# Kernel tuning notes

Measured on AMD Instinct MI355X. Metric: run time of the kernel, lower is better.

## Reference

```python
import jax, jax.numpy as jnp
import numpy as np

B, C, K = 8192, 4096, 4096
BK, BN = 1, 16          # block-sparse tile sizes (bk x bn)
KEEP = 0.3


def setup_inputs() -> dict:
    key = jax.random.key(0)
    kx, kw, kb, km = jax.random.split(key, 4)
    stdv = 1.0 / np.sqrt(C * K)  # reset_parameters uses 1/sqrt(C*K)
    x = jax.random.normal(kx, (B, C), dtype=jnp.float32)
    weight = jax.random.uniform(kw, (K, C), dtype=jnp.float32, minval=-stdv, maxval=stdv)
    # block mask on (K/bk, C/bn) grid, expanded to full weight shape
    blk = (jax.random.uniform(km, (K // BK, C // BN)) < KEEP).astype(jnp.float32)
    mask = jnp.repeat(jnp.repeat(blk, BK, axis=0), BN, axis=1)  # [K, C]
    weight = weight * mask
    bias = jax.random.uniform(kb, (K,), dtype=jnp.float32, minval=-stdv, maxval=stdv)
    return {"x": x, "weight": weight, "bias": bias}


def reference(x, weight, bias):
    # SparseLinearRelu forward (sparse-kernel path, attr='relu'):
    # y = relu(x @ W^T + b); zero blocks of W contribute nothing (skipped by kernel).
    return jax.nn.relu(jnp.dot(x, weight.T) + bias)
```

## Files before the change

kernel.cpp:

```cpp
#include <hip/hip_runtime.h>
#include <hip/hip_bf16.h>

typedef __attribute__((ext_vector_type(4))) float f32x4;
typedef __attribute__((ext_vector_type(8))) short bf16x8;
typedef __attribute__((ext_vector_type(4))) short bf16x4v;

#define M_DIM 8192
#define N_DIM 4096
#define K_DIM 4096
#define NX (M_DIM * K_DIM)
#define NW (N_DIM * K_DIM)

#define BM 256
#define BN 256
#define BK 64
#define NKT (K_DIM / BK)
#define THREADS 512

#define GLOAD_LDS16(g, l)                                                        \
  __builtin_amdgcn_global_load_lds(                                              \
      (const __attribute__((address_space(1))) void*)(g),                        \
      (__attribute__((address_space(3))) void*)(l), 16, 0, 0)

__global__ __launch_bounds__(256) void convert_bf16(const float* __restrict__ x,
                                                    const float* __restrict__ w,
                                                    short* __restrict__ ws) {
  const long stride = (long)gridDim.x * blockDim.x;
  const long total8 = ((long)NX + NW) / 8;
  for (long i = blockIdx.x * (long)blockDim.x + threadIdx.x; i < total8; i += stride) {
    const long base = i * 8;
    const float* src = (base < NX) ? (x + base) : (w + (base - NX));
    short* dst = ws + base;
    f32x4 a = *(const f32x4*)src;
    f32x4 b = *(const f32x4*)(src + 4);
    bf16x8 o;
    o[0] = (short)__bfloat16_as_ushort(__float2bfloat16(a[0]));
    o[1] = (short)__bfloat16_as_ushort(__float2bfloat16(a[1]));
    o[2] = (short)__bfloat16_as_ushort(__float2bfloat16(a[2]));
    o[3] = (short)__bfloat16_as_ushort(__float2bfloat16(a[3]));
    o[4] = (short)__bfloat16_as_ushort(__float2bfloat16(b[0]));
    o[5] = (short)__bfloat16_as_ushort(__float2bfloat16(b[1]));
    o[6] = (short)__bfloat16_as_ushort(__float2bfloat16(b[2]));
    o[7] = (short)__bfloat16_as_ushort(__float2bfloat16(b[3]));
    *(bf16x8*)dst = o;
  }
}

__global__ __launch_bounds__(THREADS, 2) void gemm256_bf16(
    const short* __restrict__ Abf,
    const short* __restrict__ Bbf,
    const float* __restrict__ bias,
    float* __restrict__ Y) {
  __shared__ short lds[2 * 32768];
  char* const ldsb = (char*)lds;

  const int tid  = threadIdx.x;
  const int lane = tid & 63;
  const int wave = tid >> 6;
  const int wm   = wave >> 2;
  const int wn   = wave & 3;

  const int lin = blockIdx.x + blockIdx.y * (N_DIM / BN);
  const int swz = (lin & 7) * 64 + (lin >> 3);
  const int bx = swz & 15;
  const int by = swz >> 4;
  const long rowA0 = (long)by * BM;
  const long rowB0 = (long)bx * BN;

  const int sg_col = (((lane & 7) ^ ((lane >> 3) & 7)) << 3);
  const int s_row  = wave * 8 + (lane >> 3);
  const int voff = s_row * K_DIM + sg_col;

  const short* uA = Abf + rowA0 * (long)K_DIM;
  const short* uB = Bbf + rowB0 * (long)K_DIM;

  const int offk0 = (lane & 15) * 128 + ((((lane >> 4)) ^ (lane & 7)) << 4);
  const int offk1 = (lane & 15) * 128 + (((4 + (lane >> 4)) ^ (lane & 7)) << 4);

#define STAGE_HALF(BOFF_, HALF_, TT) do {                                        \
    const short* u_ = ((HALF_) < 2 ? uA : uB) +                                  \
                      (long)(((HALF_) & 1) * 128) * K_DIM + (long)(TT) * BK;     \
    char* l_ = ldsb + (BOFF_) + ((HALF_) < 2 ? 0 : 32768) +                      \
               ((HALF_) & 1) * 16384 + wave * 1024;                              \
    GLOAD_LDS16(u_ + voff, l_);                                                  \
    GLOAD_LDS16(u_ + 64 * K_DIM + voff, l_ + 8192);                              \
  } while (0)

#define PH_READ_A(DST, BOFF_, MADD) do {                                         \
    const char* pa_ = ldsb + (BOFF_) + wm * 16384 + (MADD);                      \
    _Pragma("unroll")                                                            \
    for (int m_ = 0; m_ < 4; ++m_) {                                             \
      DST[m_][0] = *(const bf16x8*)(pa_ + m_ * 2048 + offk0);                    \
      DST[m_][1] = *(const bf16x8*)(pa_ + m_ * 2048 + offk1);                    \
    }                                                                            \
  } while (0)

#define PH_READ_B(DST, BOFF_, NADD) do {                                         \
    const char* pb_ = ldsb + (BOFF_) + 32768 + wn * 8192 + (NADD);               \
    _Pragma("unroll")                                                            \
    for (int n_ = 0; n_ < 2; ++n_) {                                             \
      DST[n_][0] = *(const bf16x8*)(pb_ + n_ * 2048 + offk0);                    \
      DST[n_][1] = *(const bf16x8*)(pb_ + n_ * 2048 + offk1);                    \
    }                                                                            \
  } while (0)

#define MFMA16(AF, BF, MB, NB) do {                                              \
    __builtin_amdgcn_s_setprio(1);                                               \
    _Pragma("unroll")                                                            \
    for (int kk_ = 0; kk_ < 2; ++kk_)                                            \
      _Pragma("unroll")                                                          \
      for (int m_ = 0; m_ < 4; ++m_)                                             \
        _Pragma("unroll")                                                        \
        for (int n_ = 0; n_ < 2; ++n_)                                           \
          acc[(MB) + m_][(NB) + n_] = __builtin_amdgcn_mfma_f32_16x16x32_bf16(   \
              AF[m_][kk_], BF[n_][kk_], acc[(MB) + m_][(NB) + n_], 0, 0, 0);     \
    __builtin_amdgcn_s_setprio(0);                                               \
  } while (0)

#define TILE(BOFF_, T, DO_ST, VM) do {                                           \
                               \
    PH_READ_A(af, BOFF_, 0);                                                     \
    PH_READ_B(bfr01, BOFF_, 0);                                                  \
    MFMA16(af, bfr01, 0, 0);                                                     \
    __builtin_amdgcn_s_barrier();                                                \
                                        \
    PH_READ_B(bfr23, BOFF_, 4096);                                               \
    MFMA16(af, bfr23, 0, 2);                                                     \
    __builtin_amdgcn_s_barrier();                                                \
                                        \
    PH_READ_A(af, BOFF_, 8192);                                                  \
    MFMA16(af, bfr01, 4, 0);                                                     \
    __builtin_amdgcn_s_barrier();                                                \
               \
    if (DO_ST) {                                                                 \
      STAGE_HALF(BOFF_, 0, (T) + 2);                                             \
      STAGE_HALF(BOFF_, 1, (T) + 2);                                             \
      STAGE_HALF(BOFF_, 2, (T) + 2);                                             \
      STAGE_HALF(BOFF_, 3, (T) + 2);                                             \
    }                                                                            \
    MFMA16(af, bfr23, 4, 2);                                                     \
    if ((VM) == 8)      asm volatile("s_waitcnt vmcnt(8)" ::: "memory");         \
    else if ((VM) == 0) asm volatile("s_waitcnt vmcnt(0)" ::: "memory");         \
    if ((VM) >= 0) __builtin_amdgcn_s_barrier();                                 \
  } while (0)

  f32x4 acc[8][4];
#pragma unroll
  for (int i = 0; i < 8; ++i)
#pragma unroll
    for (int j = 0; j < 4; ++j) acc[i][j] = (f32x4)0.0f;

  bf16x8 af[4][2], bfr01[2][2], bfr23[2][2];

  STAGE_HALF(0, 0, 0);
  STAGE_HALF(0, 1, 0);
  STAGE_HALF(0, 2, 0);
  STAGE_HALF(0, 3, 0);
  STAGE_HALF(65536, 0, 1);
  STAGE_HALF(65536, 1, 1);
  STAGE_HALF(65536, 2, 1);
  STAGE_HALF(65536, 3, 1);
  asm volatile("s_waitcnt vmcnt(8)" ::: "memory");
  __builtin_amdgcn_s_barrier();

  for (int tp = 0; tp < NKT / 2 - 1; ++tp) {
    const int t0 = 2 * tp;
    TILE(0,     t0,     1, 8);
    TILE(65536, t0 + 1, 1, 8);
  }
  TILE(0,     NKT - 2, 0, 0);
  TILE(65536, NKT - 1, 0, -1);

#undef TILE
#undef MFMA16
#undef PH_READ_B
#undef PH_READ_A
#undef STAGE_HALF

  const int c0 = lane & 15;
  const int r0 = (lane >> 4) * 4;
#pragma unroll
  for (int j = 0; j < 4; ++j) {
    const long gc = rowB0 + wn * 64 + j * 16 + c0;
    const float bv = bias[gc];
#pragma unroll
    for (int i = 0; i < 8; ++i) {
      const long gr0 = rowA0 + wm * 128 + i * 16 + r0;
#pragma unroll
      for (int r = 0; r < 4; ++r) {
        float v = acc[i][j][r] + bv;
        Y[(gr0 + r) * (long)N_DIM + gc] = fmaxf(v, 0.0f);
      }
    }
  }
}

#define FBM 128
#define FBK 32
#define FLDSS 40
__global__ __launch_bounds__(256) void fallback_gemm(
    const float* __restrict__ X, const float* __restrict__ W,
    const float* __restrict__ bias, float* __restrict__ Y) {
  __shared__ short As[FBM * FLDSS];
  __shared__ short Bs[FBM * FLDSS];
  const int tid = threadIdx.x, lane = tid & 63, wave = tid >> 6;
  const int wm = (wave >> 1) * 64, wn = (wave & 1) * 64;
  const long rowA0 = (long)blockIdx.y * FBM, rowB0 = (long)blockIdx.x * FBM;
  const int srow = tid >> 3, scol = (tid & 7) * 4;
  const float* Aptr = X + (rowA0 + srow) * (long)K_DIM + scol;
  const float* Bptr = W + (rowB0 + srow) * (long)K_DIM + scol;
  f32x4 ra[4], rb[4];
#pragma unroll
  for (int i = 0; i < 4; ++i) {
    ra[i] = *(const f32x4*)(Aptr + (long)i * 32 * K_DIM);
    rb[i] = *(const f32x4*)(Bptr + (long)i * 32 * K_DIM);
  }
  f32x4 acc[4][4];
#pragma unroll
  for (int i = 0; i < 4; ++i)
#pragma unroll
    for (int j = 0; j < 4; ++j) acc[i][j] = (f32x4)0.0f;
  for (int kt = 0; kt < K_DIM / FBK; ++kt) {
    __syncthreads();
#pragma unroll
    for (int i = 0; i < 4; ++i) {
      bf16x4v pa, pb;
#pragma unroll
      for (int j = 0; j < 4; ++j) {
        pa[j] = (short)__bfloat16_as_ushort(__float2bfloat16(ra[i][j]));
        pb[j] = (short)__bfloat16_as_ushort(__float2bfloat16(rb[i][j]));
      }
      *(bf16x4v*)&As[(i * 32 + srow) * FLDSS + scol] = pa;
      *(bf16x4v*)&Bs[(i * 32 + srow) * FLDSS + scol] = pb;
    }
    if (kt + 1 < K_DIM / FBK) {
      const float* An = Aptr + (kt + 1) * FBK;
      const float* Bn = Bptr + (kt + 1) * FBK;
#pragma unroll
      for (int i = 0; i < 4; ++i) {
        ra[i] = *(const f32x4*)(An + (long)i * 32 * K_DIM);
        rb[i] = *(const f32x4*)(Bn + (long)i * 32 * K_DIM);
      }
    }
    __syncthreads();
    bf16x8 af[4], bfr[4];
#pragma unroll
    for (int i = 0; i < 4; ++i) {
      af[i]  = *(const bf16x8*)&As[(wm + i * 16 + (lane & 15)) * FLDSS + (lane >> 4) * 8];
      bfr[i] = *(const bf16x8*)&Bs[(wn + i * 16 + (lane & 15)) * FLDSS + (lane >> 4) * 8];
    }
#pragma unroll
    for (int i = 0; i < 4; ++i)
#pragma unroll
      for (int j = 0; j < 4; ++j)
        acc[i][j] = __builtin_amdgcn_mfma_f32_16x16x32_bf16(af[i], bfr[j], acc[i][j], 0, 0, 0);
  }
  const int r0 = (lane >> 4) * 4, c0 = lane & 15;
#pragma unroll
  for (int j = 0; j < 4; ++j) {
    const long gc = rowB0 + wn + j * 16 + c0;
    const float bv = bias[gc];
#pragma unroll
    for (int i = 0; i < 4; ++i) {
      const long gr0 = rowA0 + wm + i * 16 + r0;
#pragma unroll
      for (int r = 0; r < 4; ++r) {
        float v = acc[i][j][r] + bv;
        Y[(gr0 + r) * (long)N_DIM + gc] = fmaxf(v, 0.0f);
      }
    }
  }
}

extern "C" void kernel_launch(void* const* d_in, const int* in_sizes, int n_in,
                              void* d_out, int out_size, void* d_ws, size_t ws_size,
                              hipStream_t stream) {
  const float* x = (const float*)d_in[0];
  const float* w = (const float*)d_in[1];
  const float* b = (const float*)d_in[2];
  float* y = (float*)d_out;

  const size_t need = (size_t)(NX + NW) * sizeof(short);
  if (ws_size >= need) {
    short* ws = (short*)d_ws;
    convert_bf16<<<2048, 256, 0, stream>>>(x, w, ws);
    dim3 grid(N_DIM / BN, M_DIM / BM);
    gemm256_bf16<<<grid, dim3(THREADS), 0, stream>>>(ws, ws + NX, b, y);
  } else {
    dim3 grid(N_DIM / FBM, M_DIM / FBM);
    fallback_gemm<<<grid, dim3(256), 0, stream>>>(x, w, b, y);
  }
}
```

Baseline: 296.5 us.

## Switch main GEMM to 32x32x16 bf16 MFMA with reworked fragment reads

Replaces the 16x16x32 MFMA tiling with 32x32x16 MFMA instructions. LDS fragment offsets, A/B register fragments, the accumulator layout and the epilogue store mapping are all changed to match. The global-to-LDS staging for the next tile is split across two phases of the tile loop instead of being issued all at once. Larger MFMA tiles cut the LDS reads per FLOP and the instruction count, but the new swizzled offsets may cause bank conflicts, and the 32x32 output layout makes the epilogue stores more scattered.

```diff
diff --git a/kernel.cpp b/kernel.cpp
--- a/kernel.cpp
+++ b/kernel.cpp
@@ -2,6 +2,7 @@
 #include <hip/hip_bf16.h>
 
 typedef __attribute__((ext_vector_type(4))) float f32x4;
+typedef __attribute__((ext_vector_type(16))) float f32x16;
 typedef __attribute__((ext_vector_type(8))) short bf16x8;
 typedef __attribute__((ext_vector_type(4))) short bf16x4v;
 
@@ -74,8 +75,10 @@
   const short* uA = Abf + rowA0 * (long)K_DIM;
   const short* uB = Bbf + rowB0 * (long)K_DIM;
 
-  const int offk0 = (lane & 15) * 128 + ((((lane >> 4)) ^ (lane & 7)) << 4);
-  const int offk1 = (lane & 15) * 128 + (((4 + (lane >> 4)) ^ (lane & 7)) << 4);
+  int offs[4];
+#pragma unroll
+  for (int s = 0; s < 4; ++s)
+    offs[s] = (lane & 31) * 128 + ((((2 * s) | (lane >> 5)) ^ (lane & 7)) << 4);
 
 #define STAGE_HALF(BOFF_, HALF_, TT) do {                                        \
     const short* u_ = ((HALF_) < 2 ? uA : uB) +                                  \
@@ -86,71 +89,63 @@
     GLOAD_LDS16(u_ + 64 * K_DIM + voff, l_ + 8192);                              \
   } while (0)
 
-#define PH_READ_A(DST, BOFF_, MADD) do {                                         \
-    const char* pa_ = ldsb + (BOFF_) + wm * 16384 + (MADD);                      \
+#define READ_A2(DST, BOFF_, MTB) do {                                            \
+    const char* pa_ = ldsb + (BOFF_) + wm * 16384 + (MTB) * 4096;                \
     _Pragma("unroll")                                                            \
-    for (int m_ = 0; m_ < 4; ++m_) {                                             \
-      DST[m_][0] = *(const bf16x8*)(pa_ + m_ * 2048 + offk0);                    \
-      DST[m_][1] = *(const bf16x8*)(pa_ + m_ * 2048 + offk1);                    \
-    }                                                                            \
-  } while (0)
-
-#define PH_READ_B(DST, BOFF_, NADD) do {                                         \
-    const char* pb_ = ldsb + (BOFF_) + 32768 + wn * 8192 + (NADD);               \
+    for (int mt_ = 0; mt_ < 2; ++mt_)                                            \
+      _Pragma("unroll")                                                          \
+      for (int s_ = 0; s_ < 4; ++s_)                                             \
+        DST[mt_][s_] = *(const bf16x8*)(pa_ + mt_ * 4096 + offs[s_]);            \
+  } while (0)
+
+#define READ_B1(DST, BOFF_, NT) do {                                             \
+    const char* pb_ = ldsb + (BOFF_) + 32768 + wn * 8192 + (NT) * 4096;          \
     _Pragma("unroll")                                                            \
-    for (int n_ = 0; n_ < 2; ++n_) {                                             \
-      DST[n_][0] = *(const bf16x8*)(pb_ + n_ * 2048 + offk0);                    \
-      DST[n_][1] = *(const bf16x8*)(pb_ + n_ * 2048 + offk1);                    \
-    }                                                                            \
-  } while (0)
-
-#define MFMA16(AF, BF, MB, NB) do {                                              \
+    for (int s_ = 0; s_ < 4; ++s_)                                               \
+      DST[s_] = *(const bf16x8*)(pb_ + offs[s_]);                                \
+  } while (0)
+
+#define MFMA8(AF2, BF, MT0, NT) do {                                             \
     __builtin_amdgcn_s_setprio(1);                                               \
     _Pragma("unroll")                                                            \
-    for (int kk_ = 0; kk_ < 2; ++kk_)                                            \
+    for (int s_ = 0; s_ < 4; ++s_)                                               \
       _Pragma("unroll")                                                          \
-      for (int m_ = 0; m_ < 4; ++m_)                                             \
-        _Pragma("unroll")                                                        \
-        for (int n_ = 0; n_ < 2; ++n_)                                           \
-          acc[(MB) + m_][(NB) + n_] = __builtin_amdgcn_mfma_f32_16x16x32_bf16(   \
-              AF[m_][kk_], BF[n_][kk_], acc[(MB) + m_][(NB) + n_], 0, 0, 0);     \
+      for (int mt_ = 0; mt_ < 2; ++mt_)                                          \
+        acc[(MT0) + mt_][NT] = __builtin_amdgcn_mfma_f32_32x32x16_bf16(          \
+            AF2[mt_][s_], BF[s_], acc[(MT0) + mt_][NT], 0, 0, 0);                \
     __builtin_amdgcn_s_setprio(0);                                               \
   } while (0)
 
 #define TILE(BOFF_, T, DO_ST, VM) do {                                           \
                                \
-    PH_READ_A(af, BOFF_, 0);                                                     \
-    PH_READ_B(bfr01, BOFF_, 0);                                                  \
-    MFMA16(af, bfr01, 0, 0);                                                     \
+    READ_A2(af01, BOFF_, 0);                                                     \
+    READ_B1(bf0, BOFF_, 0);                                                      \
+    MFMA8(af01, bf0, 0, 0);                                                      \
     __builtin_amdgcn_s_barrier();                                                \
-                                        \
-    PH_READ_B(bfr23, BOFF_, 4096);                                               \
-    MFMA16(af, bfr23, 0, 2);                                                     \
+                                       \
+    READ_A2(af23, BOFF_, 2);                                                     \
+    MFMA8(af23, bf0, 2, 0);                                                      \
     __builtin_amdgcn_s_barrier();                                                \
-                                        \
-    PH_READ_A(af, BOFF_, 8192);                                                  \
-    MFMA16(af, bfr01, 4, 0);                                                     \
+                           \
+    READ_B1(bf1, BOFF_, 1);                                                      \
+    if (DO_ST) { STAGE_HALF(BOFF_, 0, (T) + 2); STAGE_HALF(BOFF_, 1, (T) + 2); } \
+    MFMA8(af23, bf1, 2, 1);                                                      \
     __builtin_amdgcn_s_barrier();                                                \
-               \
-    if (DO_ST) {                                                                 \
-      STAGE_HALF(BOFF_, 0, (T) + 2);                                             \
-      STAGE_HALF(BOFF_, 1, (T) + 2);                                             \
-      STAGE_HALF(BOFF_, 2, (T) + 2);                                             \
-      STAGE_HALF(BOFF_, 3, (T) + 2);                                             \
-    }                                                                            \
-    MFMA16(af, bfr23, 4, 2);                                                     \
+                   \
+    if (DO_ST) { STAGE_HALF(BOFF_, 2, (T) + 2); STAGE_HALF(BOFF_, 3, (T) + 2); } \
+    MFMA8(af01, bf1, 0, 1);                                                      \
     if ((VM) == 8)      asm volatile("s_waitcnt vmcnt(8)" ::: "memory");         \
     else if ((VM) == 0) asm volatile("s_waitcnt vmcnt(0)" ::: "memory");         \
     if ((VM) >= 0) __builtin_amdgcn_s_barrier();                                 \
   } while (0)
 
-  f32x4 acc[8][4];
-#pragma unroll
-  for (int i = 0; i < 8; ++i)
-#pragma unroll
-    for (int j = 0; j < 4; ++j) acc[i][j] = (f32x4)0.0f;
-
-  bf16x8 af[4][2], bfr01[2][2], bfr23[2][2];
+  f32x16 acc[4][2];
+#pragma unroll
+  for (int i = 0; i < 4; ++i)
+#pragma unroll
+    for (int j = 0; j < 2; ++j) acc[i][j] = (f32x16)0.0f;
+
+  bf16x8 af01[2][4], af23[2][4], bf0[4], bf1[4];
 
   STAGE_HALF(0, 0, 0);
   STAGE_HALF(0, 1, 0);
@@ -172,24 +167,25 @@
   TILE(65536, NKT - 1, 0, -1);
 
 #undef TILE
-#undef MFMA16
-#undef PH_READ_B
-#undef PH_READ_A
+#undef MFMA8
+#undef READ_B1
+#undef READ_A2
 #undef STAGE_HALF
 
-  const int c0 = lane & 15;
-  const int r0 = (lane >> 4) * 4;
-#pragma unroll
-  for (int j = 0; j < 4; ++j) {
-    const long gc = rowB0 + wn * 64 + j * 16 + c0;
+  const int c0 = lane & 31;
+  const int r0 = 4 * (lane >> 5);
+#pragma unroll
+  for (int nt = 0; nt < 2; ++nt) {
+    const long gc = rowB0 + wn * 64 + nt * 32 + c0;
     const float bv = bias[gc];
 #pragma unroll
-    for (int i = 0; i < 8; ++i) {
-      const long gr0 = rowA0 + wm * 128 + i * 16 + r0;
-#pragma unroll
-      for (int r = 0; r < 4; ++r) {
-        float v = acc[i][j][r] + bv;
-        Y[(gr0 + r) * (long)N_DIM + gc] = fmaxf(v, 0.0f);
+    for (int mt = 0; mt < 4; ++mt) {
+      const long gr0 = rowA0 + wm * 128 + mt * 32 + r0;
+#pragma unroll
+      for (int r = 0; r < 16; ++r) {
+        const long gr = gr0 + (r & 3) + 8 * (r >> 2);
+        float v = acc[mt][nt][r] + bv;
+        Y[gr * (long)N_DIM + gc] = fmaxf(v, 0.0f);
       }
     }
   }
```

New measurement: 283.9 us. -4.3%, faster.

## Split next-tile staging across phases and vectorize epilogue stores via LDS transpose

Applied to the files above, without the earlier changes.

The global-to-LDS staging of the tile two steps ahead is split in two. Half is issued after the second A-fragment read and half just before the last MFMA group, which spreads memory traffic across the compute phases. The prologue staging order is changed to match. The epilogue now routes each wave's accumulators through a per-wave LDS scratch area so lanes can write 16-byte row-contiguous float4 stores with a vectorized bias add, replacing scattered 4-byte stores. This trades extra LDS traffic and some scratch reuse risk for fewer, better-coalesced global writes.

```diff
diff --git a/kernel.cpp b/kernel.cpp
--- a/kernel.cpp
+++ b/kernel.cpp
@@ -127,17 +127,13 @@
     PH_READ_B(bfr23, BOFF_, 4096);                                               \
     MFMA16(af, bfr23, 0, 2);                                                     \
     __builtin_amdgcn_s_barrier();                                                \
-                                        \
+                          \
     PH_READ_A(af, BOFF_, 8192);                                                  \
+    if (DO_ST) { STAGE_HALF(BOFF_, 2, (T) + 2); STAGE_HALF(BOFF_, 3, (T) + 2); } \
     MFMA16(af, bfr01, 4, 0);                                                     \
     __builtin_amdgcn_s_barrier();                                                \
-               \
-    if (DO_ST) {                                                                 \
-      STAGE_HALF(BOFF_, 0, (T) + 2);                                             \
-      STAGE_HALF(BOFF_, 1, (T) + 2);                                             \
-      STAGE_HALF(BOFF_, 2, (T) + 2);                                             \
-      STAGE_HALF(BOFF_, 3, (T) + 2);                                             \
-    }                                                                            \
+                   \
+    if (DO_ST) { STAGE_HALF(BOFF_, 0, (T) + 2); STAGE_HALF(BOFF_, 1, (T) + 2); } \
     MFMA16(af, bfr23, 4, 2);                                                     \
     if ((VM) == 8)      asm volatile("s_waitcnt vmcnt(8)" ::: "memory");         \
     else if ((VM) == 0) asm volatile("s_waitcnt vmcnt(0)" ::: "memory");         \
@@ -156,10 +152,10 @@
   STAGE_HALF(0, 1, 0);
   STAGE_HALF(0, 2, 0);
   STAGE_HALF(0, 3, 0);
+  STAGE_HALF(65536, 2, 1);
+  STAGE_HALF(65536, 3, 1);
   STAGE_HALF(65536, 0, 1);
   STAGE_HALF(65536, 1, 1);
-  STAGE_HALF(65536, 2, 1);
-  STAGE_HALF(65536, 3, 1);
   asm volatile("s_waitcnt vmcnt(8)" ::: "memory");
   __builtin_amdgcn_s_barrier();
 
@@ -177,19 +173,35 @@
 #undef PH_READ_A
 #undef STAGE_HALF
 
-  const int c0 = lane & 15;
-  const int r0 = (lane >> 4) * 4;
-#pragma unroll
-  for (int j = 0; j < 4; ++j) {
-    const long gc = rowB0 + wn * 64 + j * 16 + c0;
-    const float bv = bias[gc];
-#pragma unroll
-    for (int i = 0; i < 8; ++i) {
-      const long gr0 = rowA0 + wm * 128 + i * 16 + r0;
-#pragma unroll
-      for (int r = 0; r < 4; ++r) {
-        float v = acc[i][j][r] + bv;
-        Y[(gr0 + r) * (long)N_DIM + gc] = fmaxf(v, 0.0f);
+  {
+    char* scr = ldsb + wave * 8192;
+    const int c0 = lane & 15;
+    const int r0 = (lane >> 4) * 4;
+    const int rd_row = lane >> 3;
+    const int rd_ch  = (lane & 7) * 16;
+#pragma unroll
+    for (int jp = 0; jp < 2; ++jp) {
+      const long gcb = rowB0 + wn * 64 + jp * 32 + (lane & 7) * 4;
+      const f32x4 bv4 = *(const f32x4*)&bias[gcb];
+#pragma unroll
+      for (int i = 0; i < 8; ++i) {
+#pragma unroll
+        for (int r = 0; r < 4; ++r) {
+          *(float*)(scr + (r0 + r) * 144 + c0 * 4)      = acc[i][2 * jp + 0][r];
+          *(float*)(scr + (r0 + r) * 144 + 64 + c0 * 4) = acc[i][2 * jp + 1][r];
+        }
+        f32x4 v0 = *(const f32x4*)(scr + rd_row * 144 + rd_ch);
+        f32x4 v1 = *(const f32x4*)(scr + (8 + rd_row) * 144 + rd_ch);
+        v0 += bv4;
+        v1 += bv4;
+#pragma unroll
+        for (int e = 0; e < 4; ++e) {
+          v0[e] = fmaxf(v0[e], 0.0f);
+          v1[e] = fmaxf(v1[e], 0.0f);
+        }
+        const long gr = rowA0 + wm * 128 + i * 16;
+        *(f32x4*)&Y[(gr + rd_row) * (long)N_DIM + gcb]     = v0;
+        *(f32x4*)&Y[(gr + 8 + rd_row) * (long)N_DIM + gcb] = v1;
       }
     }
   }
```

Result: faster. 251.3 us (-15.3%).
